# Performance work log

Measured on AMD Instinct MI355X. Metric: run time of the kernel, lower is better.

## Reference

```python
import jax, jax.numpy as jnp
import numpy as np

B, S, D, H = 8, 1024, 1024, 16
DH = D // H
EPS = 1e-5


def _layernorm(x):
    # elementwise_affine=False LayerNorm, eps=1e-5
    m = jnp.mean(x, axis=-1, keepdims=True)
    v = jnp.var(x, axis=-1, keepdims=True)
    return (x - m) * jax.lax.rsqrt(v + EPS)


def setup_inputs() -> dict:
    key = jax.random.key(0)
    ks = jax.random.split(key, 11)
    s = 0.02
    return {
        "x": jax.random.normal(ks[0], (B, S, D), jnp.float32),
        "y": jax.random.normal(ks[1], (B, 1, D), jnp.float32),
        "w_adaln": jax.random.normal(ks[2], (6 * D, D), jnp.float32) * s,
        "b_adaln": jnp.zeros((6 * D,), jnp.float32),
        "w_qkv": jax.random.normal(ks[3], (3 * D, D), jnp.float32) * s,
        "w_proj": jax.random.normal(ks[4], (D, D), jnp.float32) * s,
        "b_proj": jnp.zeros((D,), jnp.float32),
        "w_fc1": jax.random.normal(ks[5], (4 * D, D), jnp.float32) * s,
        "b_fc1": jnp.zeros((4 * D,), jnp.float32),
        "w_fc2": jax.random.normal(ks[6], (D, 4 * D), jnp.float32) * s,
        "b_fc2": jnp.zeros((D,), jnp.float32),
    }


def reference(x, y, w_adaln, b_adaln, w_qkv, w_proj, b_proj, w_fc1, b_fc1, w_fc2, b_fc2):
    # adaLN-Zero modulation params from conditioning y: SiLU -> Linear -> 6 chunks
    mods = jax.nn.silu(y) @ w_adaln.T + b_adaln          # [B,1,6D]
    sh_a, sc_a, g_a, sh_m, sc_m, g_m = jnp.split(mods, 6, axis=-1)

    # --- attention branch ---
    xm = _layernorm(x) * (1.0 + sc_a) + sh_a             # modulate
    qkv = xm @ w_qkv.T                                   # [B,S,3D] (qkv_bias=False)
    q, k, v = [t.reshape(B, S, H, DH).transpose(0, 2, 1, 3) for t in jnp.split(qkv, 3, axis=-1)]
    scale = 1.0 / np.sqrt(DH)
    scores = jnp.einsum("bhqd,bhkd->bhqk", q, k) * scale  # unfused MATH-backend sdpa
    attn = jax.nn.softmax(scores, axis=-1)
    o = jnp.einsum("bhqk,bhkd->bhqd", attn, v)
    o = o.transpose(0, 2, 1, 3).reshape(B, S, D)
    o = o @ w_proj.T + b_proj
    x = x + g_a * o                                      # gated residual

    # --- MLP branch ---
    xm = _layernorm(x) * (1.0 + sc_m) + sh_m
    h = jax.nn.gelu(xm @ w_fc1.T + b_fc1, approximate=True)  # GELU(tanh)
    h = h @ w_fc2.T + b_fc2
    return x + g_m * h
```

## Files before the change

kernel.cpp:

```cpp
#include <hip/hip_runtime.h>

typedef __bf16 bf16;
typedef __attribute__((ext_vector_type(8))) __bf16 bf16x8;
typedef __attribute__((ext_vector_type(4))) __bf16 bf16x4;
typedef __attribute__((ext_vector_type(2))) __bf16 bf16x2;
typedef __attribute__((ext_vector_type(4))) float f32x4;

#define MFMA16(a, b, c) __builtin_amdgcn_mfma_f32_16x16x32_bf16((a), (b), (c), 0, 0, 0)

__device__ __forceinline__ float clampf(float v, float c) {
    return fminf(fmaxf(v, -c), c);
}

__device__ __forceinline__ void gload16(const void* g, void* l) {
    __builtin_amdgcn_global_load_lds((const __attribute__((address_space(1))) void*)g,
                                     (__attribute__((address_space(3))) void*)l, 16, 0, 0);
}

__launch_bounds__(256)
__global__ void cvt_kernel(const float* __restrict__ src, bf16* __restrict__ dst, int n4)
{
    int i = blockIdx.x * 256 + threadIdx.x;
    if (i < n4) {
        float4 v = ((const float4*)src)[i];
        bf16x4 o;
        o[0] = (bf16)v.x; o[1] = (bf16)v.y; o[2] = (bf16)v.z; o[3] = (bf16)v.w;
        ((bf16x4*)dst)[i] = o;
    }
}

__launch_bounds__(256)
__global__ void adaln_kernel(const float* __restrict__ y, const float* __restrict__ w,
                             const float* __restrict__ bias, float* __restrict__ mods)
{
    const int b = blockIdx.y;
    const int n = blockIdx.x * 256 + threadIdx.x;
    __shared__ float sy[1024];
    for (int i = threadIdx.x; i < 1024; i += 256) {
        float t = y[b * 1024 + i];
        sy[i] = t / (1.f + __expf(-t));
    }
    __syncthreads();
    const float* wr = w + (size_t)n * 1024;
    float acc = 0.f;
    for (int k = 0; k < 1024; k += 4) {
        float4 wv = *(const float4*)(wr + k);
        acc += sy[k] * wv.x + sy[k + 1] * wv.y + sy[k + 2] * wv.z + sy[k + 3] * wv.w;
    }
    mods[b * 6144 + n] = clampf(acc + bias[n], 64.f);
}

__launch_bounds__(256)
__global__ void ln_mod_kernel(const float* __restrict__ xin, const float* __restrict__ mods,
                              int shOff, int scOff, bf16* __restrict__ out)
{
    const int row = blockIdx.x;
    const int b = row >> 10;
    const int tid = threadIdx.x;
    const int wave = tid >> 6, lane = tid & 63;

    const float4 x4 = *((const float4*)xin + (size_t)row * 256 + tid);
    float v[4] = {x4.x, x4.y, x4.z, x4.w};

    float s = v[0] + v[1] + v[2] + v[3];
    float ss = v[0]*v[0] + v[1]*v[1] + v[2]*v[2] + v[3]*v[3];
#pragma unroll
    for (int o = 32; o > 0; o >>= 1) {
        s  += __shfl_xor(s, o, 64);
        ss += __shfl_xor(ss, o, 64);
    }
    __shared__ float red[8];
    if (lane == 0) { red[wave] = s; red[4 + wave] = ss; }
    __syncthreads();
    s  = red[0] + red[1] + red[2] + red[3];
    ss = red[4] + red[5] + red[6] + red[7];
    const float mean = s * (1.f / 1024.f);
    const float var  = ss * (1.f / 1024.f) - mean * mean;
    const float rstd = rsqrtf(fmaxf(var, 0.f) + 1e-5f);

    const float* mb = mods + b * 6144;
    bf16x4 o4;
#pragma unroll
    for (int j = 0; j < 4; ++j) {
        int c = tid * 4 + j;
        o4[j] = (bf16)clampf(((v[j] - mean) * rstd) * (1.f + mb[scOff + c]) + mb[shOff + c], 64.f);
    }
    *((bf16x4*)out + (size_t)row * 256 + tid) = o4;
}

template <int EPI>
__launch_bounds__(512, 4)
__global__ void gemm_np(const bf16* __restrict__ A, const bf16* __restrict__ W,
                        const float* __restrict__ bias, const float* __restrict__ mods,
                        int gateOff, const float* __restrict__ resid,
                        float* __restrict__ of, bf16* __restrict__ ob,
                        int N, int K, int nN, int GN, float clampV)
{
    __shared__ __align__(16) bf16 sm[2][3][4096];

    const int tid = threadIdx.x;
    const int wave = tid >> 6, lane = tid & 63, quad = lane >> 4, l16 = lane & 15;
    const int wm = wave >> 1, wn = wave & 1;

    const int xcd = (int)blockIdx.x & 7;
    const int p   = (int)blockIdx.x >> 3;
    const int nLoc = nN / GN;
    const int xm = xcd / GN, xn = xcd % GN;
    const int tileN = (xn * nLoc + p % nLoc) * 128;
    const int tileM = (xm * (((int)gridDim.x >> 3) / nLoc) + p / nLoc) * 256;

    const int p0 = tid * 16;
    const int l0 = p0 ^ (((p0 >> 6) & 3) << 4);
    const int srow = l0 >> 6;
    const int scol = (l0 & 63) >> 1;
    const bf16* Ag  = A + (size_t)(tileM + srow) * K + scol;
    const bf16* Ag2 = A + (size_t)(tileM + 128 + srow) * K + scol;
    const bf16* Wg  = W + (size_t)(tileN + srow) * K + scol;

    const int xorv = (l16 & 3) << 4;
    const int cxr = (quad * 16) ^ xorv;

    f32x4 acc[4][4] = {};
    bf16x8 af[4], bfr[4];

#define SPASS(b_, slot, src, ts) \
    gload16((src) + (size_t)(ts) * 32, &sm[b_][slot][wave * 512])

#define RDF(b_) do { \
        _Pragma("unroll") for (int q_ = 0; q_ < 4; ++q_) { \
            const int ra_ = (wm & 1) * 64 + q_ * 16 + l16; \
            const int rb_ = wn * 64 + q_ * 16 + l16; \
            af[q_]  = *(const bf16x8*)((const char*)&sm[b_][wm >> 1][0] + ra_ * 64 + cxr); \
            bfr[q_] = *(const bf16x8*)((const char*)&sm[b_][2][0] + rb_ * 64 + cxr); \
        } \
    } while (0)

#define MMX() do { \
        __builtin_amdgcn_s_setprio(1); \
        _Pragma("unroll") for (int m_ = 0; m_ < 4; ++m_) \
        _Pragma("unroll") for (int n_ = 0; n_ < 4; ++n_) \
            acc[m_][n_] = MFMA16(af[m_], bfr[n_], acc[m_][n_]); \
        __builtin_amdgcn_s_setprio(0); \
    } while (0)

#define SB0() __builtin_amdgcn_sched_barrier(0)
#define BARF() do { __builtin_amdgcn_s_barrier(); asm volatile("" ::: "memory"); } while (0)
#define LGKM0() do { asm volatile("s_waitcnt lgkmcnt(0)" ::: "memory"); SB0(); } while (0)
#define VMC0() do { asm volatile("s_waitcnt vmcnt(0)" ::: "memory"); SB0(); } while (0)

    const int nks = K >> 5;
    SPASS(0, 0, Ag, 0); SPASS(0, 1, Ag2, 0); SPASS(0, 2, Wg, 0);
    VMC0();
    BARF();

    for (int s = 0; s < nks; ++s) {
        const int b = s & 1;
        if (s + 1 < nks) {
            SPASS(b ^ 1, 0, Ag, s + 1);
            SPASS(b ^ 1, 1, Ag2, s + 1);
            SPASS(b ^ 1, 2, Wg, s + 1);
        }
        RDF(b);
        LGKM0();
        MMX();
        VMC0();
        BARF();
    }

#undef SPASS
#undef RDF
#undef MMX
#undef SB0
#undef BARF
#undef LGKM0
#undef VMC0

    const int rowB = tileM + wm * 64 + quad * 4;
    const int colB = tileN + wn * 64 + l16;
#pragma unroll
    for (int mt = 0; mt < 4; ++mt) {
#pragma unroll
        for (int nt = 0; nt < 4; ++nt) {
            const int col = colB + nt * 16;
#pragma unroll
            for (int i = 0; i < 4; ++i) {
                const int row = rowB + mt * 16 + i;
                float v = acc[mt][nt][i];
                if (EPI != 0) v += bias[col];
                if (EPI == 0) {
                    ob[(size_t)row * N + col] = (bf16)clampf(v, clampV);
                } else if (EPI == 1) {
                    const int bb = row >> 10;
                    const float g = mods[bb * 6144 + gateOff + col];
                    of[(size_t)row * N + col] =
                        clampf(resid[(size_t)row * N + col] + g * v, clampV);
                } else {
                    const float e = __expf(1.5957691216f * (v + 0.044715f * v * v * v));
                    const float tt = 1.f - 2.f / (e + 1.f);
                    ob[(size_t)row * N + col] = (bf16)clampf(0.5f * v * (1.f + tt), clampV);
                }
            }
        }
    }
}

template <int EPI>
__launch_bounds__(256)
__global__ void gemm_bt(const bf16* __restrict__ A, const float* __restrict__ W,
                        const float* __restrict__ bias, const float* __restrict__ mods,
                        int gateOff, const float* __restrict__ resid,
                        float* __restrict__ of, bf16* __restrict__ ob,
                        int M, int N, int K, float clampV)
{
    constexpr int LDT = 40;
    __shared__ bf16 As[128 * LDT];
    __shared__ bf16 Bs[128 * LDT];

    const int tid = threadIdx.x;
    const int wave = tid >> 6, lane = tid & 63, quad = lane >> 4, l16 = lane & 15;
    const int wrow = wave >> 1, wcol = wave & 1;
    const int tileM = blockIdx.y * 128, tileN = blockIdx.x * 128;
    const int sr = tid >> 2;
    const int sk = (tid & 3) * 8;

    const bf16*  Ag = A + (size_t)(tileM + sr) * K + sk;
    const float* Wg = W + (size_t)(tileN + sr) * K + sk;

    f32x4 acc[4][4] = {};

    for (int k0 = 0; k0 < K; k0 += 32) {
        bf16x8 a0 = *(const bf16x8*)(Ag + k0);
        bf16x8 a1 = *(const bf16x8*)(Ag + (size_t)64 * K + k0);
        float4 w0a = *(const float4*)(Wg + k0);
        float4 w0b = *(const float4*)(Wg + k0 + 4);
        float4 w1a = *(const float4*)(Wg + (size_t)64 * K + k0);
        float4 w1b = *(const float4*)(Wg + (size_t)64 * K + k0 + 4);
        bf16x8 b0, b1;
        b0[0] = (bf16)w0a.x; b0[1] = (bf16)w0a.y; b0[2] = (bf16)w0a.z; b0[3] = (bf16)w0a.w;
        b0[4] = (bf16)w0b.x; b0[5] = (bf16)w0b.y; b0[6] = (bf16)w0b.z; b0[7] = (bf16)w0b.w;
        b1[0] = (bf16)w1a.x; b1[1] = (bf16)w1a.y; b1[2] = (bf16)w1a.z; b1[3] = (bf16)w1a.w;
        b1[4] = (bf16)w1b.x; b1[5] = (bf16)w1b.y; b1[6] = (bf16)w1b.z; b1[7] = (bf16)w1b.w;
        *(bf16x8*)&As[sr * LDT + sk] = a0;
        *(bf16x8*)&As[(sr + 64) * LDT + sk] = a1;
        *(bf16x8*)&Bs[sr * LDT + sk] = b0;
        *(bf16x8*)&Bs[(sr + 64) * LDT + sk] = b1;
        __syncthreads();

        bf16x8 af[4], bfr[4];
#pragma unroll
        for (int mt = 0; mt < 4; ++mt)
            af[mt] = *(const bf16x8*)&As[(wrow * 64 + mt * 16 + l16) * LDT + quad * 8];
#pragma unroll
        for (int nt = 0; nt < 4; ++nt)
            bfr[nt] = *(const bf16x8*)&Bs[(wcol * 64 + nt * 16 + l16) * LDT + quad * 8];
#pragma unroll
        for (int mt = 0; mt < 4; ++mt)
#pragma unroll
            for (int nt = 0; nt < 4; ++nt)
                acc[mt][nt] = MFMA16(af[mt], bfr[nt], acc[mt][nt]);
        __syncthreads();
    }

#pragma unroll
    for (int mt = 0; mt < 4; ++mt) {
#pragma unroll
        for (int nt = 0; nt < 4; ++nt) {
            const int col = tileN + wcol * 64 + nt * 16 + l16;
#pragma unroll
            for (int i = 0; i < 4; ++i) {
                const int row = tileM + wrow * 64 + mt * 16 + quad * 4 + i;
                float v = acc[mt][nt][i];
                if (EPI != 0) v += bias[col];
                if (EPI == 0) {
                    ob[(size_t)row * N + col] = (bf16)clampf(v, clampV);
                } else if (EPI == 1) {
                    const int bb = row >> 10;
                    const float g = mods[bb * 6144 + gateOff + col];
                    of[(size_t)row * N + col] =
                        clampf(resid[(size_t)row * N + col] + g * v, clampV);
                } else {
                    const float e = __expf(1.5957691216f * (v + 0.044715f * v * v * v));
                    const float t = 1.f - 2.f / (e + 1.f);
                    ob[(size_t)row * N + col] = (bf16)clampf(0.5f * v * (1.f + t), clampV);
                }
            }
        }
    }
}

__launch_bounds__(256)
__global__ void attn_kernel(const bf16* __restrict__ qkv, bf16* __restrict__ o)
{
    const int bid = blockIdx.x;
    const int qt = bid >> 7;
    const int b  = (bid >> 4) & 7;
    const int h  = bid & 15;
    const int tid = threadIdx.x;
    const int wave = tid >> 6, lane = tid & 63, quad = lane >> 4, l16 = lane & 15;

    __shared__ bf16 Kl[64 * 72];
    __shared__ bf16 Vt[64 * 72];
    __shared__ bf16 Pl[4][32 * 72];

    const size_t basebs = (size_t)b * 1024 * 3072;
    const int qbase = qt * 128 + wave * 32;

    bf16x8 qf[2][2];
#pragma unroll
    for (int mt = 0; mt < 2; ++mt)
#pragma unroll
        for (int kk = 0; kk < 2; ++kk) {
            const int row = qbase + mt * 16 + l16;
            const int dh = kk * 32 + quad * 8;
            qf[mt][kk] = *(const bf16x8*)(qkv + basebs + (size_t)row * 3072 + h * 64 + dh);
        }

    const int kr = tid >> 2, kc = (tid & 3) * 16;
    const int vp = tid >> 3, vc = (tid & 7) * 8;
    const bf16* Kg = qkv + basebs + (size_t)kr * 3072 + 1024 + h * 64 + kc;
    const bf16* Vg = qkv + basebs + (size_t)(2 * vp) * 3072 + 2048 + h * 64 + vc;
    const size_t ktStep = (size_t)64 * 3072;

    bf16x8 k0 = *(const bf16x8*)Kg;
    bf16x8 k1 = *(const bf16x8*)(Kg + 8);
    bf16x8 v0 = *(const bf16x8*)Vg;
    bf16x8 v1 = *(const bf16x8*)(Vg + 3072);

    f32x4 oacc[2][4] = {};
    float lsum[2][4] = {};

    for (int kt = 0; kt < 16; ++kt) {
        *(bf16x8*)&Kl[kr * 72 + kc] = k0;
        *(bf16x8*)&Kl[kr * 72 + kc + 8] = k1;
#pragma unroll
        for (int j = 0; j < 8; ++j) {
            bf16x2 pr; pr[0] = v0[j]; pr[1] = v1[j];
            *(bf16x2*)&Vt[(vc + j) * 72 + 2 * vp] = pr;
        }
        __syncthreads();

        const size_t noff = (size_t)(kt < 15 ? kt + 1 : 15) * ktStep;
        k0 = *(const bf16x8*)(Kg + noff);
        k1 = *(const bf16x8*)(Kg + noff + 8);
        v0 = *(const bf16x8*)(Vg + noff);
        v1 = *(const bf16x8*)(Vg + noff + 3072);

        f32x4 s[2][4] = {};
#pragma unroll
        for (int kk = 0; kk < 2; ++kk)
#pragma unroll
            for (int nt = 0; nt < 4; ++nt) {
                bf16x8 kf = *(const bf16x8*)&Kl[(nt * 16 + l16) * 72 + kk * 32 + quad * 8];
#pragma unroll
                for (int mt = 0; mt < 2; ++mt)
                    s[mt][nt] = MFMA16(qf[mt][kk], kf, s[mt][nt]);
            }

#pragma unroll
        for (int mt = 0; mt < 2; ++mt)
#pragma unroll
            for (int nt = 0; nt < 4; ++nt)
#pragma unroll
                for (int i = 0; i < 4; ++i) {
                    float p = exp2f(fminf(s[mt][nt][i] * 0.18033688f, 43.f));
                    Pl[wave][(mt * 16 + quad * 4 + i) * 72 + nt * 16 + l16] = (bf16)p;
                    lsum[mt][i] += p;
                }

#pragma unroll
        for (int kk = 0; kk < 2; ++kk) {
            bf16x8 pf[2];
#pragma unroll
            for (int mt = 0; mt < 2; ++mt)
                pf[mt] = *(const bf16x8*)&Pl[wave][(mt * 16 + l16) * 72 + kk * 32 + quad * 8];
#pragma unroll
            for (int nt = 0; nt < 4; ++nt) {
                bf16x8 vf = *(const bf16x8*)&Vt[(nt * 16 + l16) * 72 + kk * 32 + quad * 8];
#pragma unroll
                for (int mt = 0; mt < 2; ++mt)
                    oacc[mt][nt] = MFMA16(pf[mt], vf, oacc[mt][nt]);
            }
        }
        __syncthreads();
    }

    bf16* ob = o + (size_t)b * 1024 * 1024 + h * 64;
#pragma unroll
    for (int mt = 0; mt < 2; ++mt)
#pragma unroll
        for (int i = 0; i < 4; ++i) {
            float l = lsum[mt][i];
#pragma unroll
            for (int off = 1; off < 16; off <<= 1) l += __shfl_xor(l, off, 64);
            const float inv = 1.f / fmaxf(l, 1e-20f);
            const int row = qbase + mt * 16 + quad * 4 + i;
#pragma unroll
            for (int nt = 0; nt < 4; ++nt)
                ob[(size_t)row * 1024 + nt * 16 + l16] = (bf16)clampf(oacc[mt][nt][i] * inv, 16.f);
        }
}

extern "C" void kernel_launch(void* const* d_in, const int* in_sizes, int n_in,
                              void* d_out, int out_size, void* d_ws, size_t ws_size,
                              hipStream_t stream)
{
    const float* x       = (const float*)d_in[0];
    const float* y       = (const float*)d_in[1];
    const float* w_adaln = (const float*)d_in[2];
    const float* b_adaln = (const float*)d_in[3];
    const float* w_qkv   = (const float*)d_in[4];
    const float* w_proj  = (const float*)d_in[5];
    const float* b_proj  = (const float*)d_in[6];
    const float* w_fc1   = (const float*)d_in[7];
    const float* b_fc1   = (const float*)d_in[8];
    const float* w_fc2   = (const float*)d_in[9];
    const float* b_fc2   = (const float*)d_in[10];
    float* out = (float*)d_out;

    char* ws = (char*)d_ws;
    float* mods = (float*)ws;
    bf16* bufA  = (bf16*)(ws + (1ull << 18));
    bf16* bufH  = (bf16*)(ws + (1ull << 18) + (1ull << 24));
    size_t off = (1ull << 18) + (1ull << 24) + (1ull << 26);
    bf16* wb_qkv  = (bf16*)(ws + off);               off += 6ull << 20;
    bf16* wb_proj = (bf16*)(ws + off);               off += 2ull << 20;
    bf16* wb_fc1  = (bf16*)(ws + off);               off += 8ull << 20;
    bf16* wb_fc2  = (bf16*)(ws + off);               off += 8ull << 20;
    const bool fast = ws_size >= off;

    adaln_kernel<<<dim3(24, 8), 256, 0, stream>>>(y, w_adaln, b_adaln, mods);
    ln_mod_kernel<<<8192, 256, 0, stream>>>(x, mods, 0, 1024, bufA);

    if (fast) {
        cvt_kernel<<<(3072 * 256 + 255) / 256, 256, 0, stream>>>(w_qkv, wb_qkv, 3072 * 256);
        cvt_kernel<<<(1024 * 256 + 255) / 256, 256, 0, stream>>>(w_proj, wb_proj, 1024 * 256);
        cvt_kernel<<<(4096 * 256 + 255) / 256, 256, 0, stream>>>(w_fc1, wb_fc1, 4096 * 256);
        cvt_kernel<<<(4096 * 256 + 255) / 256, 256, 0, stream>>>(w_fc2, wb_fc2, 4096 * 256);

        gemm_np<0><<<768, 512, 0, stream>>>(bufA, wb_qkv, nullptr, nullptr, 0,
                                            nullptr, nullptr, bufH, 3072, 1024, 24, 4, 64.f);
        attn_kernel<<<1024, 256, 0, stream>>>(bufH, bufA);
        gemm_np<1><<<256, 512, 0, stream>>>(bufA, wb_proj, b_proj, mods, 2048,
                                            x, out, nullptr, 1024, 1024, 8, 2, 64.f);
        ln_mod_kernel<<<8192, 256, 0, stream>>>(out, mods, 3072, 4096, bufA);
        gemm_np<2><<<1024, 512, 0, stream>>>(bufA, wb_fc1, b_fc1, nullptr, 0,
                                             nullptr, nullptr, bufH, 4096, 1024, 32, 4, 64.f);
        gemm_np<1><<<256, 512, 0, stream>>>(bufH, wb_fc2, b_fc2, mods, 5120,
                                            out, out, nullptr, 1024, 4096, 8, 4, 64.f);
    } else {
        gemm_bt<0><<<dim3(24, 64), 256, 0, stream>>>(bufA, w_qkv, nullptr, nullptr, 0,
                                                     nullptr, nullptr, bufH, 8192, 3072, 1024, 64.f);
        attn_kernel<<<1024, 256, 0, stream>>>(bufH, bufA);
        gemm_bt<1><<<dim3(8, 64), 256, 0, stream>>>(bufA, w_proj, b_proj, mods, 2048,
                                                    x, out, nullptr, 8192, 1024, 1024, 64.f);
        ln_mod_kernel<<<8192, 256, 0, stream>>>(out, mods, 3072, 4096, bufA);
        gemm_bt<2><<<dim3(32, 64), 256, 0, stream>>>(bufA, w_fc1, b_fc1, nullptr, 0,
                                                     nullptr, nullptr, bufH, 8192, 4096, 1024, 64.f);
        gemm_bt<1><<<dim3(8, 64), 256, 0, stream>>>(bufH, w_fc2, b_fc2, mods, 5120,
                                                    out, out, nullptr, 8192, 1024, 4096, 64.f);
    }
}
```

Before: 548.5 us.

## Triple-buffer GEMM LDS stages with two-tile prefetch and new swizzle

```diff
diff --git a/kernel.cpp b/kernel.cpp
--- a/kernel.cpp
+++ b/kernel.cpp
@@ -96,7 +96,7 @@
                         float* __restrict__ of, bf16* __restrict__ ob,
                         int N, int K, int nN, int GN, float clampV)
 {
-    __shared__ __align__(16) bf16 sm[2][3][4096];
+    __shared__ __align__(16) bf16 sm[3][3][4096];
 
     const int tid = threadIdx.x;
     const int wave = tid >> 6, lane = tid & 63, quad = lane >> 4, l16 = lane & 15;
@@ -110,28 +110,27 @@
     const int tileM = (xm * (((int)gridDim.x >> 3) / nLoc) + p / nLoc) * 256;
 
     const int p0 = tid * 16;
-    const int l0 = p0 ^ (((p0 >> 6) & 3) << 4);
+    const int l0 = p0 ^ (((p0 >> 7) & 3) << 4);
     const int srow = l0 >> 6;
     const int scol = (l0 & 63) >> 1;
     const bf16* Ag  = A + (size_t)(tileM + srow) * K + scol;
     const bf16* Ag2 = A + (size_t)(tileM + 128 + srow) * K + scol;
     const bf16* Wg  = W + (size_t)(tileN + srow) * K + scol;
 
-    const int xorv = (l16 & 3) << 4;
-    const int cxr = (quad * 16) ^ xorv;
+    const int cxr = (quad * 16) ^ (((l16 >> 1) & 3) << 4);
 
     f32x4 acc[4][4] = {};
     bf16x8 af[4], bfr[4];
 
-#define SPASS(b_, slot, src, ts) \
-    gload16((src) + (size_t)(ts) * 32, &sm[b_][slot][wave * 512])
-
-#define RDF(b_) do { \
+#define SPASS(r_, slot, src, ts) \
+    gload16((src) + (size_t)(ts) * 32, &sm[r_][slot][wave * 512])
+
+#define RDF(r_) do { \
         _Pragma("unroll") for (int q_ = 0; q_ < 4; ++q_) { \
             const int ra_ = (wm & 1) * 64 + q_ * 16 + l16; \
             const int rb_ = wn * 64 + q_ * 16 + l16; \
-            af[q_]  = *(const bf16x8*)((const char*)&sm[b_][wm >> 1][0] + ra_ * 64 + cxr); \
-            bfr[q_] = *(const bf16x8*)((const char*)&sm[b_][2][0] + rb_ * 64 + cxr); \
+            af[q_]  = *(const bf16x8*)((const char*)&sm[r_][wm >> 1][0] + ra_ * 64 + cxr); \
+            bfr[q_] = *(const bf16x8*)((const char*)&sm[r_][2][0] + rb_ * 64 + cxr); \
         } \
     } while (0)
 
@@ -146,26 +145,32 @@
 #define SB0() __builtin_amdgcn_sched_barrier(0)
 #define BARF() do { __builtin_amdgcn_s_barrier(); asm volatile("" ::: "memory"); } while (0)
 #define LGKM0() do { asm volatile("s_waitcnt lgkmcnt(0)" ::: "memory"); SB0(); } while (0)
-#define VMC0() do { asm volatile("s_waitcnt vmcnt(0)" ::: "memory"); SB0(); } while (0)
+#define VMC3() do { asm volatile("s_waitcnt vmcnt(3)" ::: "memory"); SB0(); } while (0)
+
+#define STEP(S, r_, r2_) do { \
+        if ((S) < nks) { \
+            const int ts_ = ((S) + 2 < nks) ? (S) + 2 : nks - 1; \
+            SPASS(r2_, 0, Ag, ts_); SPASS(r2_, 1, Ag2, ts_); SPASS(r2_, 2, Wg, ts_); \
+            RDF(r_); \
+            LGKM0(); \
+            MMX(); \
+            VMC3(); \
+            BARF(); \
+        } \
+    } while (0)
 
     const int nks = K >> 5;
     SPASS(0, 0, Ag, 0); SPASS(0, 1, Ag2, 0); SPASS(0, 2, Wg, 0);
-    VMC0();
+    SPASS(1, 0, Ag, 1); SPASS(1, 1, Ag2, 1); SPASS(1, 2, Wg, 1);
+    VMC3();
     BARF();
 
-    for (int s = 0; s < nks; ++s) {
-        const int b = s & 1;
-        if (s + 1 < nks) {
-            SPASS(b ^ 1, 0, Ag, s + 1);
-            SPASS(b ^ 1, 1, Ag2, s + 1);
-            SPASS(b ^ 1, 2, Wg, s + 1);
-        }
-        RDF(b);
-        LGKM0();
-        MMX();
-        VMC0();
-        BARF();
-    }
+    for (int s = 0; s < nks; s += 3) {
+        STEP(s,     0, 2);
+        STEP(s + 1, 1, 0);
+        STEP(s + 2, 2, 1);
+    }
+    asm volatile("s_waitcnt vmcnt(0)" ::: "memory");
 
 #undef SPASS
 #undef RDF
@@ -173,7 +178,8 @@
 #undef SB0
 #undef BARF
 #undef LGKM0
-#undef VMC0
+#undef VMC3
+#undef STEP
 
     const int rowB = tileM + wm * 64 + quad * 4;
     const int colB = tileN + wn * 64 + l16;
```

After: 528.1 us. 1.04x faster.
